# Kernel optimization log

Measured on AMD Instinct MI355X. Metric: run time of the kernel, lower is better.

## Reference

```python
import jax, jax.numpy as jnp
import numpy as np

CONF_THRES = 0.4
IOU_THRES = 0.45
MAX_DET = 1000
MAX_WH = 7680.0  # class offset for non-agnostic NMS (yolov5 convention)
K = 2048         # pre-NMS candidate cap (>= MAX_DET)


def setup_inputs() -> dict:
    key = jax.random.key(0)
    k1, k2, k3, k4 = jax.random.split(key, 4)
    # uint8-valued image, stored as int32 (values 0..255)
    img = jax.random.randint(k1, (640, 640, 3), 0, 256, dtype=jnp.int32)
    B, N, NC = 8, 25200, 80
    xy = jax.random.uniform(k2, (B, N, 2)) * 640.0          # box centers in pixels
    wh = jax.random.uniform(k3, (B, N, 2)) * 80.0 + 4.0     # box sizes
    sc = jax.random.uniform(k4, (B, N, 1 + NC))             # objectness + class scores
    pred = jnp.concatenate([xy, wh, sc], axis=-1)           # [B, N, 85]
    return {"img": img, "pred": pred}


def _xywh2xyxy(x):
    xy, wh = x[..., :2], x[..., 2:4]
    return jnp.concatenate([xy - wh * 0.5, xy + wh * 0.5], axis=-1)


def _box_iou(a, b):
    # a: [K,4], b: [K,4] in xyxy
    lt = jnp.maximum(a[:, None, :2], b[None, :, :2])
    rb = jnp.minimum(a[:, None, 2:], b[None, :, 2:])
    wh = jnp.clip(rb - lt, 0.0)
    inter = wh[..., 0] * wh[..., 1]
    area_a = (a[:, 2] - a[:, 0]) * (a[:, 3] - a[:, 1])
    area_b = (b[:, 2] - b[:, 0]) * (b[:, 3] - b[:, 1])
    return inter / (area_a[:, None] + area_b[None, :] - inter + 1e-7)


def _nms_single(p):
    # p: [N, 5+nc]
    boxes = _xywh2xyxy(p[:, :4])                 # [N,4]
    conf_all = p[:, 5:] * p[:, 4:5]              # obj * cls
    conf = jnp.max(conf_all, axis=-1)            # best-class confidence [N]
    cls = jnp.argmax(conf_all, axis=-1).astype(p.dtype)
    scores = jnp.where(conf > CONF_THRES, conf, -1.0)
    # top-K candidates (score-sorted, padding gets score -1)
    top_s, idx = jax.lax.top_k(scores, K)
    b = boxes[idx]                               # [K,4] raw boxes
    c = cls[idx]                                 # [K] class ids (float)
    b_off = b + (c * MAX_WH)[:, None]            # class-offset boxes (agnostic_nms=False)
    iou = _box_iou(b_off, b_off)                 # [K,K]
    keep = top_s > CONF_THRES
    ar = jnp.arange(K)

    def body(i, keep):
        sup = keep[i] & (iou[i] > IOU_THRES) & (ar > i)
        return keep & jnp.logical_not(sup)

    keep = jax.lax.fori_loop(0, K, body, keep)
    fs = jnp.where(keep, top_s, -1.0)
    sel_s, sel = jax.lax.top_k(fs, MAX_DET)
    det = jnp.concatenate([b[sel], sel_s[:, None], c[sel][:, None]], axis=-1)  # [MAX_DET,6]
    return jnp.where((sel_s > CONF_THRES)[:, None], det, 0.0)


def reference(img, pred):
    # process_image: HWC -> CHW, BGR->RGB flip, float, /255, add batch dim
    x = img.astype(jnp.float32).transpose(2, 0, 1)[::-1] / 255.0
    x = x[None]                                  # [1,3,640,640]
    det = jax.vmap(_nms_single)(pred)[0]         # non_max_suppression(pred, ...)[0]
    return det, x
```

## Files before the change

kernel.cpp:

```cpp
#include <hip/hip_runtime.h>
#include <stdint.h>

#define N_ANCH 25200
#define NCLS   80
#define KSEL   2048
#define MAXDET 1000
#define CONF_T 0.4f
#define IOU_T  0.45f
#define MAX_WH 7680.0f
#define HBINS  512
#define HBASE  0xBE00u
#define NCAND_MAX 4096
#define NSB    788
#define NIB    1200
#define SUPCAP 224

#define WS_SELSCORE  0
#define WS_SELBOX    8192
#define WS_DETCAND   40960
#define WS_HIST      90112
#define WS_CNT       92160
#define WS_KEYS      92480
#define WS_CLS       193280
#define WS_MASK      294912
#define WS_FLAGS     819200
#define WS_CAND      294912

__global__ void __launch_bounds__(256)
prep_kernel(const float* __restrict__ pred0, uint32_t* __restrict__ keys,
            int* __restrict__ cls, uint32_t* __restrict__ ghist) {
    int tid = threadIdx.x;
    int lane = tid & 63, wave = tid >> 6;
    int g = lane >> 3, l = lane & 7;
    int a = blockIdx.x * 32 + wave * 8 + g;
    if (a >= N_ANCH) return;
    const float* p = pred0 + (size_t)a * 85;
    float obj = p[4];
    float v = -1e30f; int ci = 0;
    #pragma unroll
    for (int k = 0; k < 10; ++k) {
        int c = l + 8 * k;
        float x = p[5 + c] * obj;
        if (x > v) { v = x; ci = c; }
    }
    #pragma unroll
    for (int m = 1; m < 8; m <<= 1) {
        float ov = __shfl_xor(v, m, 64);
        int   oc = __shfl_xor(ci, m, 64);
        if (ov > v || (ov == v && oc < ci)) { v = ov; ci = oc; }
    }
    if (l == 0) {
        float score = (v > CONF_T) ? v : -1.0f;
        uint32_t bits = __float_as_uint(score);
        uint32_t key = (bits & 0x80000000u) ? ~bits : (bits | 0x80000000u);
        keys[a] = key; cls[a] = ci;
        if (key >= (HBASE << 16)) atomicAdd(&ghist[(key >> 16) - HBASE], 1u);
    }
}

__global__ void __launch_bounds__(256)
compact_kernel(const uint32_t* __restrict__ keys, const uint32_t* __restrict__ ghist,
               uint32_t* __restrict__ cnt, unsigned long long* __restrict__ cand,
               const int* __restrict__ img, float* __restrict__ xout) {
    __shared__ uint32_t h[HBINS];
    __shared__ uint32_t s_lim;
    __shared__ int wtot[4];
    __shared__ int s_base;
    int tid = threadIdx.x;

    if (blockIdx.x >= 25) {
        int b = blockIdx.x - 25;
        int i4  = b * 1024 + tid * 4;
        int c   = i4 / 409600;
        int rem = i4 - c * 409600;
        int ch  = 2 - c;
        const int4* im4 = (const int4*)(img + (size_t)rem * 3);
        int4 v0 = im4[0], v1 = im4[1], v2 = im4[2];
        int p0 = (ch == 0) ? v0.x : (ch == 1) ? v0.y : v0.z;
        int p1 = (ch == 0) ? v0.w : (ch == 1) ? v1.x : v1.y;
        int p2 = (ch == 0) ? v1.z : (ch == 1) ? v1.w : v2.x;
        int p3 = (ch == 0) ? v2.y : (ch == 1) ? v2.z : v2.w;
        float4 o;
        o.x = (float)p0 / 255.0f; o.y = (float)p1 / 255.0f;
        o.z = (float)p2 / 255.0f; o.w = (float)p3 / 255.0f;
        *(float4*)(xout + i4) = o;
        return;
    }

    int lane = tid & 63, wv = tid >> 6;
    h[tid] = ghist[tid]; h[tid + 256] = ghist[tid + 256];
    if (tid == 0) s_lim = (HBASE << 16);
    __syncthreads();
    for (int off = 1; off < HBINS; off <<= 1) {
        uint32_t a0 = h[tid] + ((tid + off < HBINS) ? h[tid + off] : 0u);
        uint32_t a1 = h[tid + 256] + ((tid + 256 + off < HBINS) ? h[tid + 256 + off] : 0u);
        __syncthreads();
        h[tid] = a0; h[tid + 256] = a1;
        __syncthreads();
    }
    for (int b = tid; b < HBINS; b += 256) {
        uint32_t sb  = h[b];
        uint32_t sb1 = (b < HBINS - 1) ? h[b + 1] : 0u;
        if (sb >= KSEL && sb1 < KSEL) s_lim = (uint32_t)(HBASE + b) << 16;
    }
    __syncthreads();
    uint32_t lim = s_lim;

    int i = blockIdx.x * 256 + tid;
    bool valid = (i < N_ANCH / 4);
    uint32_t ks[4] = {0, 0, 0, 0};
    int cm = 0;
    if (valid) {
        uint4 kk = ((const uint4*)keys)[i];
        ks[0] = kk.x; ks[1] = kk.y; ks[2] = kk.z; ks[3] = kk.w;
        #pragma unroll
        for (int j = 0; j < 4; ++j) cm += (ks[j] >= lim) ? 1 : 0;
    }
    int pre = cm;
    #pragma unroll
    for (int o = 1; o < 64; o <<= 1) {
        int v = __shfl_up(pre, o, 64);
        if (lane >= o) pre += v;
    }
    if (lane == 63) wtot[wv] = pre;
    __syncthreads();
    if (tid == 0) {
        int t = 0;
        #pragma unroll
        for (int w = 0; w < 4; ++w) { int x = wtot[w]; wtot[w] = t; t += x; }
        s_base = (t > 0) ? (int)atomicAdd(cnt, (uint32_t)t) : 0;
    }
    __syncthreads();
    int pos = s_base + wtot[wv] + (pre - cm);
    if (valid) {
        #pragma unroll
        for (int j = 0; j < 4; ++j) {
            if (ks[j] >= lim) {
                if (pos < NCAND_MAX)
                    cand[pos] = ((unsigned long long)ks[j] << 32)
                              | (uint32_t)(~(uint32_t)(i * 4 + j));
                ++pos;
            }
        }
    }
}

__global__ void __launch_bounds__(256)
rank_kernel(const uint32_t* __restrict__ cnt, const unsigned long long* __restrict__ cand,
            const float* __restrict__ pred0, const int* __restrict__ cls,
            float* __restrict__ sel_score, float4* __restrict__ selbox,
            float* __restrict__ det_cand) {
    __shared__ unsigned long long s_it[NCAND_MAX];
    __shared__ int s_n;
    int tid = threadIdx.x;
    if (tid == 0) s_n = (int)min(*cnt, (uint32_t)NCAND_MAX);
    __syncthreads();
    int n = s_n;
    int base = blockIdx.x * 32;
    if (base >= n) return;
    for (int i = tid; i < n; i += 256) s_it[i] = cand[i];
    __syncthreads();
    int grp = tid >> 4, s16 = tid & 15;
    #pragma unroll
    for (int o = 0; o < 2; ++o) {
        int it = base + grp + o * 16;
        if (it >= n) break;
        unsigned long long mine = s_it[it];
        int c = 0;
        for (int t = s16; t < n; t += 16)
            c += (s_it[t] > mine) ? 1 : 0;
        #pragma unroll
        for (int m = 1; m < 16; m <<= 1) c += __shfl_xor(c, m, 64);
        if (s16 == 0 && c < KSEL) {
            uint32_t key = (uint32_t)(mine >> 32);
            int ai = (int)(~(uint32_t)mine);
            uint32_t fb = (key & 0x80000000u) ? (key & 0x7FFFFFFFu) : ~key;
            float score = __uint_as_float(fb);
            const float* p = pred0 + (size_t)ai * 85;
            float x = p[0], y = p[1], w = p[2], hh = p[3];
            float x1 = x - w * 0.5f, y1 = y - hh * 0.5f;
            float x2 = x + w * 0.5f, y2 = y + hh * 0.5f;
            float cf = (float)cls[ai];
            float off = cf * MAX_WH;
            selbox[c] = make_float4(x1 + off, y1 + off, x2 + off, y2 + off);
            float* dc = det_cand + (size_t)c * 6;
            dc[0] = x1; dc[1] = y1; dc[2] = x2; dc[3] = y2; dc[4] = score; dc[5] = cf;
            sel_score[c] = score;
        }
    }
}

__global__ void __launch_bounds__(256)
mask_kernel(const float4* __restrict__ selbox, uint32_t* __restrict__ MT,
            uint32_t* __restrict__ flags) {
    __shared__ float4 jb[32];
    int tid = threadIdx.x;
    int lane = tid & 63, wv = tid >> 6;
    int wi = blockIdx.x >> 3, rg = blockIdx.x & 7;

    if (tid < 32) jb[tid] = selbox[wi * 32 + tid];
    __syncthreads();
    int row = rg * 256 + tid;
    float4 a = selbox[row];
    float areaA = (a.z - a.x) * (a.w - a.y);
    uint32_t bits = 0;
    #pragma unroll 4
    for (int b = 0; b < 32; ++b) {
        int j = wi * 32 + b;
        if (j > row) {
            float4 q = jb[b];
            float lx = fmaxf(a.x, q.x), ly = fmaxf(a.y, q.y);
            float rx = fminf(a.z, q.z), ry = fminf(a.w, q.w);
            float ww = fmaxf(rx - lx, 0.0f), hh = fmaxf(ry - ly, 0.0f);
            float inter = ww * hh;
            float areaB = (q.z - q.x) * (q.w - q.y);
            float iou = inter / (areaA + areaB - inter + 1e-7f);
            if (iou > IOU_T) bits |= (1u << b);
        }
    }
    MT[(size_t)wi * 2048 + row] = bits;
    unsigned long long bm = __ballot(bits != 0u);
    if (lane == 0) {
        int wbase = wi * 64 + rg * 8 + wv * 2;
        flags[wbase]     = (uint32_t)bm;
        flags[wbase + 1] = (uint32_t)(bm >> 32);
    }
}

__global__ void __launch_bounds__(256)
nms_kernel(const uint32_t* __restrict__ MT, const uint32_t* __restrict__ flags,
           const float* __restrict__ sel_score,
           const float* __restrict__ det_cand, float* __restrict__ det) {
    __shared__ uint32_t f[64];
    __shared__ int rowlist[SUPCAP];
    __shared__ uint32_t sup[SUPCAP * 64];
    __shared__ int s_R;
    int tid = threadIdx.x;

    if (tid < 64) {
        uint32_t fw = 0;
        for (int wi = 0; wi < 64; ++wi)
            fw |= flags[wi * 64 + tid];
        f[tid] = fw;
        int cnt = __popc(fw);
        int pre = cnt;
        for (int o = 1; o < 64; o <<= 1) {
            int v = __shfl_up(pre, o, 64);
            if (tid >= o) pre += v;
        }
        int r = pre - cnt;
        while (fw) {
            int b = __ffs(fw) - 1; fw &= fw - 1;
            if (r < SUPCAP) rowlist[r] = tid * 32 + b;
            ++r;
        }
        if (tid == 63) s_R = pre;
    }
    __syncthreads();
    int R = s_R;
    bool sparse = (R <= SUPCAP);
    if (sparse) {
        for (int s = tid >> 6; s < R; s += 4)
            sup[s * 64 + (tid & 63)] = MT[(size_t)(tid & 63) * 2048 + rowlist[s]];
    }
    __syncthreads();
    if (tid >= 64) return;

    int lane = tid;
    uint32_t removed = 0;
    #pragma unroll
    for (int b = 0; b < 32; ++b)
        if (!(sel_score[lane * 32 + b] > CONF_T)) removed |= (1u << b);

    if (sparse) {
        int slot = 0;
        for (int w = 0; w < 64; ++w) {
            uint32_t fb = f[w];
            while (fb) {
                int b = __ffs(fb) - 1; fb &= fb - 1;
                uint32_t rv = __shfl((int)removed, w, 64);
                if (!((rv >> b) & 1u))
                    removed |= sup[slot * 64 + lane];
                ++slot;
            }
        }
    } else {
        for (int c = 0; c < 64; ++c) {
            const uint4* mb = (const uint4*)(MT + (size_t)lane * 2048 + c * 32);
            uint4 qa[8];
            #pragma unroll
            for (int k = 0; k < 8; ++k) qa[k] = mb[k];
            uint32_t rw[32];
            #pragma unroll
            for (int k = 0; k < 8; ++k) {
                rw[4*k] = qa[k].x; rw[4*k+1] = qa[k].y;
                rw[4*k+2] = qa[k].z; rw[4*k+3] = qa[k].w;
            }
            uint32_t keptmask = 0;
            if (lane == c) {
                uint32_t myrem = removed;
                #pragma unroll
                for (int b = 0; b < 32; ++b)
                    if (!((myrem >> b) & 1u)) { keptmask |= (1u << b); myrem |= rw[b]; }
            }
            keptmask = __shfl(keptmask, c, 64);
            #pragma unroll
            for (int b = 0; b < 32; ++b)
                if ((keptmask >> b) & 1u) removed |= rw[b];
        }
    }

    uint32_t kw = ~removed;
    int cnt2 = __popc(kw);
    int pre = cnt2;
    for (int o = 1; o < 64; o <<= 1) {
        int v = __shfl_up(pre, o, 64);
        if (lane >= o) pre += v;
    }
    int excl = pre - cnt2;
    int total = __shfl(pre, 63, 64);

    int r = excl;
    for (int b = 0; b < 32; ++b) {
        if ((kw >> b) & 1u) {
            if (r < MAXDET) {
                const float* src = det_cand + (size_t)(lane * 32 + b) * 6;
                float* dst = det + (size_t)r * 6;
                for (int j = 0; j < 6; ++j) dst[j] = src[j];
            }
            ++r;
        }
    }
    int start = total < MAXDET ? total : MAXDET;
    for (int z = start + lane; z < MAXDET; z += 64) {
        float* dst = det + (size_t)z * 6;
        for (int j = 0; j < 6; ++j) dst[j] = 0.0f;
    }
}

extern "C" void kernel_launch(void* const* d_in, const int* in_sizes, int n_in,
                              void* d_out, int out_size, void* d_ws, size_t ws_size,
                              hipStream_t stream) {
    const int*   img  = (const int*)d_in[0];
    const float* pred = (const float*)d_in[1];
    float* out = (float*)d_out;
    char* ws = (char*)d_ws;

    float*    sel_score = (float*)(ws + WS_SELSCORE);
    float4*   selbox    = (float4*)(ws + WS_SELBOX);
    float*    det_cand  = (float*)(ws + WS_DETCAND);
    uint32_t* ghist     = (uint32_t*)(ws + WS_HIST);
    uint32_t* cnt       = (uint32_t*)(ws + WS_CNT);
    uint32_t* keys      = (uint32_t*)(ws + WS_KEYS);
    int*      cls       = (int*)(ws + WS_CLS);
    uint32_t* MT        = (uint32_t*)(ws + WS_MASK);
    uint32_t* flags     = (uint32_t*)(ws + WS_FLAGS);
    unsigned long long* cand = (unsigned long long*)(ws + WS_CAND);

    hipMemsetAsync(ghist, 0, 2052, stream);
    prep_kernel<<<NSB, 256, 0, stream>>>(pred, keys, cls, ghist);
    compact_kernel<<<25 + NIB, 256, 0, stream>>>(keys, ghist, cnt, cand,
                                                 img, out + MAXDET * 6);
    rank_kernel<<<128, 256, 0, stream>>>(cnt, cand, pred, cls,
                                         sel_score, selbox, det_cand);
    mask_kernel<<<512, 256, 0, stream>>>(selbox, MT, flags);
    nms_kernel<<<1, 256, 0, stream>>>(MT, flags, sel_score, det_cand, out);
}
```

Before: 165.3 us.

## Drop memset and global histogram atomics, add transposed mask and atomic flags

```diff
diff --git a/kernel.cpp b/kernel.cpp
--- a/kernel.cpp
+++ b/kernel.cpp
@@ -12,24 +12,29 @@
 #define HBASE  0xBE00u
 #define NCAND_MAX 4096
 #define NSB    788
-#define NIB    1200
+#define NIB    400
 #define SUPCAP 224
 
 #define WS_SELSCORE  0
 #define WS_SELBOX    8192
 #define WS_DETCAND   40960
-#define WS_HIST      90112
 #define WS_CNT       92160
 #define WS_KEYS      92480
 #define WS_CLS       193280
 #define WS_MASK      294912
-#define WS_FLAGS     819200
+#define WS_MTT       819200
+#define WS_F         1343488
 #define WS_CAND      294912
 
 __global__ void __launch_bounds__(256)
 prep_kernel(const float* __restrict__ pred0, uint32_t* __restrict__ keys,
-            int* __restrict__ cls, uint32_t* __restrict__ ghist) {
-    int tid = threadIdx.x;
+            int* __restrict__ cls, uint32_t* __restrict__ cnt,
+            uint32_t* __restrict__ fglob) {
+    int tid = threadIdx.x;
+    if (blockIdx.x == 0) {
+        if (tid < 64) fglob[tid] = 0u;
+        if (tid == 64) *cnt = 0u;
+    }
     int lane = tid & 63, wave = tid >> 6;
     int g = lane >> 3, l = lane & 7;
     int a = blockIdx.x * 32 + wave * 8 + g;
@@ -54,13 +59,12 @@
         uint32_t bits = __float_as_uint(score);
         uint32_t key = (bits & 0x80000000u) ? ~bits : (bits | 0x80000000u);
         keys[a] = key; cls[a] = ci;
-        if (key >= (HBASE << 16)) atomicAdd(&ghist[(key >> 16) - HBASE], 1u);
-    }
-}
-
-__global__ void __launch_bounds__(256)
-compact_kernel(const uint32_t* __restrict__ keys, const uint32_t* __restrict__ ghist,
-               uint32_t* __restrict__ cnt, unsigned long long* __restrict__ cand,
+    }
+}
+
+__global__ void __launch_bounds__(256)
+compact_kernel(const uint32_t* __restrict__ keys, uint32_t* __restrict__ cnt,
+               unsigned long long* __restrict__ cand,
                const int* __restrict__ img, float* __restrict__ xout) {
     __shared__ uint32_t h[HBINS];
     __shared__ uint32_t s_lim;
@@ -69,27 +73,33 @@
     int tid = threadIdx.x;
 
     if (blockIdx.x >= 25) {
-        int b = blockIdx.x - 25;
-        int i4  = b * 1024 + tid * 4;
-        int c   = i4 / 409600;
-        int rem = i4 - c * 409600;
-        int ch  = 2 - c;
-        const int4* im4 = (const int4*)(img + (size_t)rem * 3);
-        int4 v0 = im4[0], v1 = im4[1], v2 = im4[2];
-        int p0 = (ch == 0) ? v0.x : (ch == 1) ? v0.y : v0.z;
-        int p1 = (ch == 0) ? v0.w : (ch == 1) ? v1.x : v1.y;
-        int p2 = (ch == 0) ? v1.z : (ch == 1) ? v1.w : v2.x;
-        int p3 = (ch == 0) ? v2.y : (ch == 1) ? v2.z : v2.w;
-        float4 o;
-        o.x = (float)p0 / 255.0f; o.y = (float)p1 / 255.0f;
-        o.z = (float)p2 / 255.0f; o.w = (float)p3 / 255.0f;
-        *(float4*)(xout + i4) = o;
+        int i = (blockIdx.x - 25) * 256 + tid;
+        const int4* im4 = (const int4*)(img + (size_t)i * 12);
+        int4 va = im4[0], vb = im4[1], vc = im4[2];
+        int p0 = i * 4;
+        float4 o0 = make_float4((float)va.z / 255.0f, (float)vb.y / 255.0f,
+                                (float)vc.x / 255.0f, (float)vc.w / 255.0f);
+        float4 o1 = make_float4((float)va.y / 255.0f, (float)vb.x / 255.0f,
+                                (float)vb.w / 255.0f, (float)vc.z / 255.0f);
+        float4 o2 = make_float4((float)va.x / 255.0f, (float)va.w / 255.0f,
+                                (float)vb.z / 255.0f, (float)vc.y / 255.0f);
+        *(float4*)(xout + p0)          = o0;
+        *(float4*)(xout + 409600 + p0) = o1;
+        *(float4*)(xout + 819200 + p0) = o2;
         return;
     }
 
     int lane = tid & 63, wv = tid >> 6;
-    h[tid] = ghist[tid]; h[tid + 256] = ghist[tid + 256];
+    for (int b = tid; b < HBINS; b += 256) h[b] = 0u;
     if (tid == 0) s_lim = (HBASE << 16);
+    __syncthreads();
+    for (int i = tid; i < N_ANCH / 4; i += 256) {
+        uint4 kk = ((const uint4*)keys)[i];
+        if (kk.x >= (HBASE << 16)) atomicAdd(&h[(kk.x >> 16) - HBASE], 1u);
+        if (kk.y >= (HBASE << 16)) atomicAdd(&h[(kk.y >> 16) - HBASE], 1u);
+        if (kk.z >= (HBASE << 16)) atomicAdd(&h[(kk.z >> 16) - HBASE], 1u);
+        if (kk.w >= (HBASE << 16)) atomicAdd(&h[(kk.w >> 16) - HBASE], 1u);
+    }
     __syncthreads();
     for (int off = 1; off < HBINS; off <<= 1) {
         uint32_t a0 = h[tid] + ((tid + off < HBINS) ? h[tid + off] : 0u);
@@ -192,7 +202,7 @@
 
 __global__ void __launch_bounds__(256)
 mask_kernel(const float4* __restrict__ selbox, uint32_t* __restrict__ MT,
-            uint32_t* __restrict__ flags) {
+            uint32_t* __restrict__ MTT, uint32_t* __restrict__ fglob) {
     __shared__ float4 jb[32];
     int tid = threadIdx.x;
     int lane = tid & 63, wv = tid >> 6;
@@ -219,17 +229,19 @@
         }
     }
     MT[(size_t)wi * 2048 + row] = bits;
+    MTT[(size_t)row * 64 + wi] = bits;
     unsigned long long bm = __ballot(bits != 0u);
     if (lane == 0) {
-        int wbase = wi * 64 + rg * 8 + wv * 2;
-        flags[wbase]     = (uint32_t)bm;
-        flags[wbase + 1] = (uint32_t)(bm >> 32);
-    }
-}
-
-__global__ void __launch_bounds__(256)
-nms_kernel(const uint32_t* __restrict__ MT, const uint32_t* __restrict__ flags,
-           const float* __restrict__ sel_score,
+        int wbase = rg * 8 + wv * 2;
+        uint32_t lo = (uint32_t)bm, hi = (uint32_t)(bm >> 32);
+        if (lo) atomicOr(&fglob[wbase], lo);
+        if (hi) atomicOr(&fglob[wbase + 1], hi);
+    }
+}
+
+__global__ void __launch_bounds__(256)
+nms_kernel(const uint32_t* __restrict__ MT, const uint32_t* __restrict__ MTT,
+           const uint32_t* __restrict__ fglob, const float* __restrict__ sel_score,
            const float* __restrict__ det_cand, float* __restrict__ det) {
     __shared__ uint32_t f[64];
     __shared__ int rowlist[SUPCAP];
@@ -238,9 +250,7 @@
     int tid = threadIdx.x;
 
     if (tid < 64) {
-        uint32_t fw = 0;
-        for (int wi = 0; wi < 64; ++wi)
-            fw |= flags[wi * 64 + tid];
+        uint32_t fw = fglob[tid];
         f[tid] = fw;
         int cnt = __popc(fw);
         int pre = cnt;
@@ -261,7 +271,7 @@
     bool sparse = (R <= SUPCAP);
     if (sparse) {
         for (int s = tid >> 6; s < R; s += 4)
-            sup[s * 64 + (tid & 63)] = MT[(size_t)(tid & 63) * 2048 + rowlist[s]];
+            sup[s * 64 + (tid & 63)] = MTT[(size_t)rowlist[s] * 64 + (tid & 63)];
     }
     __syncthreads();
     if (tid >= 64) return;
@@ -349,20 +359,19 @@
     float*    sel_score = (float*)(ws + WS_SELSCORE);
     float4*   selbox    = (float4*)(ws + WS_SELBOX);
     float*    det_cand  = (float*)(ws + WS_DETCAND);
-    uint32_t* ghist     = (uint32_t*)(ws + WS_HIST);
     uint32_t* cnt       = (uint32_t*)(ws + WS_CNT);
     uint32_t* keys      = (uint32_t*)(ws + WS_KEYS);
     int*      cls       = (int*)(ws + WS_CLS);
     uint32_t* MT        = (uint32_t*)(ws + WS_MASK);
-    uint32_t* flags     = (uint32_t*)(ws + WS_FLAGS);
+    uint32_t* MTT       = (uint32_t*)(ws + WS_MTT);
+    uint32_t* fglob     = (uint32_t*)(ws + WS_F);
     unsigned long long* cand = (unsigned long long*)(ws + WS_CAND);
 
-    hipMemsetAsync(ghist, 0, 2052, stream);
-    prep_kernel<<<NSB, 256, 0, stream>>>(pred, keys, cls, ghist);
-    compact_kernel<<<25 + NIB, 256, 0, stream>>>(keys, ghist, cnt, cand,
+    prep_kernel<<<NSB, 256, 0, stream>>>(pred, keys, cls, cnt, fglob);
+    compact_kernel<<<25 + NIB, 256, 0, stream>>>(keys, cnt, cand,
                                                  img, out + MAXDET * 6);
     rank_kernel<<<128, 256, 0, stream>>>(cnt, cand, pred, cls,
                                          sel_score, selbox, det_cand);
-    mask_kernel<<<512, 256, 0, stream>>>(selbox, MT, flags);
-    nms_kernel<<<1, 256, 0, stream>>>(MT, flags, sel_score, det_cand, out);
-}
+    mask_kernel<<<512, 256, 0, stream>>>(selbox, MT, MTT, fglob);
+    nms_kernel<<<1, 256, 0, stream>>>(MT, MTT, fglob, sel_score, det_cand, out);
+}
```

Result: faster. 148.0 us (-10.5%).
